# Performance work log

Hardware: AMD Instinct MI355X
Metric: run time of the kernel (lower is better)

## Reference

```python
import jax, jax.numpy as jnp
import numpy as np

ALPHA_F, GAMMA_F = 0.25, 2.0   # focal loss params
SMOOTH = 1e-6                  # dice smooth
THETA = 5.0                    # boundary weight
W_FOCAL, W_DICE, W_BOUND = 0.3, 0.4, 0.3


def _erode(m):
    # one iteration of scipy binary_erosion, cross (connectivity-1) structure,
    # border_value=0 (outside treated as False)
    p = jnp.pad(m, ((0, 0), (0, 0), (1, 1), (1, 1)), constant_values=False)
    c = p[:, :, 1:-1, 1:-1]
    up = p[:, :, :-2, 1:-1]
    dn = p[:, :, 2:, 1:-1]
    lf = p[:, :, 1:-1, :-2]
    rt = p[:, :, 1:-1, 2:]
    return c & up & dn & lf & rt


def _dilate(m):
    # one iteration of scipy binary_dilation, cross structure, border_value=0
    p = jnp.pad(m, ((0, 0), (0, 0), (1, 1), (1, 1)), constant_values=False)
    c = p[:, :, 1:-1, 1:-1]
    up = p[:, :, :-2, 1:-1]
    dn = p[:, :, 2:, 1:-1]
    lf = p[:, :, 1:-1, :-2]
    rt = p[:, :, 1:-1, 2:]
    return c | up | dn | lf | rt


def setup_inputs() -> dict:
    key = jax.random.key(0)
    k1, k2 = jax.random.split(key)
    B, C, H, W = 64, 1, 512, 512
    inputs = jax.random.normal(k1, (B, C, H, W), dtype=jnp.float32)
    targets = jax.random.randint(k2, (B, C, H, W), 0, 2).astype(jnp.float32)
    return {"inputs": inputs, "targets": targets}


def reference(inputs, targets):
    # numerically stable BCE-with-logits, elementwise
    bce = jnp.maximum(inputs, 0.0) - inputs * targets + jnp.log1p(jnp.exp(-jnp.abs(inputs)))

    # --- focal loss ---
    pt = jnp.exp(-bce)
    focal_loss = jnp.mean(ALPHA_F * (1.0 - pt) ** GAMMA_F * bce)

    # --- dice loss ---
    p = jax.nn.sigmoid(inputs)
    intersection = jnp.sum(p * targets)
    dice = (2.0 * intersection + SMOOTH) / (jnp.sum(p) + jnp.sum(targets) + SMOOTH)
    dice_loss = 1.0 - dice

    # --- boundary-weighted BCE ---
    mask = targets > 0.5
    eroded = _erode(_erode(mask))      # iterations=2
    dilated = _dilate(_dilate(mask))   # iterations=2
    boundary = dilated & (~eroded)
    weights = boundary.astype(jnp.float32) * THETA + 1.0
    boundary_loss = jnp.mean(bce * weights)

    return W_FOCAL * focal_loss + W_DICE * dice_loss + W_BOUND * boundary_loss
```

## Files before the change

### kernel.cpp

```cpp
#include <hip/hip_runtime.h>
#include <math.h>

static constexpr int Hdim = 512;
static constexpr int Wdim = 512;
static constexpr int HW   = Hdim * Wdim;
static constexpr int NIMG = 64;
static constexpr int WPR  = Wdim / 64;
static constexpr int WPI  = Hdim * WPR;
static constexpr int TOTAL_WORDS = NIMG * WPI;
static constexpr int NBLK_A = 2048;
static constexpr int GROUPS_PER_WAVE = 8;
static constexpr int NBLK_B = TOTAL_WORDS / 256;
static constexpr int NBLK_C = 2048;
static constexpr int CTHREADS = NBLK_C * 256;
static constexpr int F4TOTAL = NIMG * HW / 4;
static constexpr int CITERS = F4TOTAL / CTHREADS;


typedef unsigned long long ull;

__device__ __forceinline__ ull spread4(ull x) {
    x = (x | (x << 24)) & 0x000000FF000000FFULL;
    x = (x | (x << 12)) & 0x000F000F000F000FULL;
    x = (x | (x << 6))  & 0x0303030303030303ULL;
    x = (x | (x << 3))  & 0x1111111111111111ULL;
    return x;
}

__global__ __launch_bounds__(256) void mask_kernel(
    const float* __restrict__ tgt, ull* __restrict__ mask)
{
    const int lane = threadIdx.x & 63;
    const int wid  = (blockIdx.x * 256 + threadIdx.x) >> 6;
    const float4* t4 = (const float4*)tgt;
    #pragma unroll
    for (int g = 0; g < GROUPS_PER_WAVE; g++) {
        const int gg = wid * GROUPS_PER_WAVE + g;
        float4 v = t4[gg * 64 + lane];
        ull b0 = __ballot(v.x > 0.5f);
        ull b1 = __ballot(v.y > 0.5f);
        ull b2 = __ballot(v.z > 0.5f);
        ull b3 = __ballot(v.w > 0.5f);
        ull w0 =  spread4( b0        & 0xFFFF)       | (spread4( b1        & 0xFFFF) << 1)
               | (spread4( b2        & 0xFFFF) << 2) | (spread4( b3        & 0xFFFF) << 3);
        ull w1 =  spread4((b0 >> 16) & 0xFFFF)       | (spread4((b1 >> 16) & 0xFFFF) << 1)
               | (spread4((b2 >> 16) & 0xFFFF) << 2) | (spread4((b3 >> 16) & 0xFFFF) << 3);
        ull w2 =  spread4((b0 >> 32) & 0xFFFF)       | (spread4((b1 >> 32) & 0xFFFF) << 1)
               | (spread4((b2 >> 32) & 0xFFFF) << 2) | (spread4((b3 >> 32) & 0xFFFF) << 3);
        ull w3 =  spread4((b0 >> 48) & 0xFFFF)       | (spread4((b1 >> 48) & 0xFFFF) << 1)
               | (spread4((b2 >> 48) & 0xFFFF) << 2) | (spread4((b3 >> 48) & 0xFFFF) << 3);
        if (lane < 4) {
            ull val = (lane == 0) ? w0 : (lane == 1) ? w1 : (lane == 2) ? w2 : w3;
            mask[gg * 4 + lane] = val;
        }
    }
}

__device__ __forceinline__ ull shl1(ull c, ull l) { return (c << 1) | (l >> 63); }
__device__ __forceinline__ ull shr1(ull c, ull r) { return (c >> 1) | (r << 63); }
__device__ __forceinline__ ull shl2(ull c, ull l) { return (c << 2) | (l >> 62); }
__device__ __forceinline__ ull shr2(ull c, ull r) { return (c >> 2) | (r << 62); }

__global__ __launch_bounds__(256) void boundary_kernel(
    const ull* __restrict__ mask, ull* __restrict__ comb)
{
    const int w = blockIdx.x * 256 + threadIdx.x;
    const int word = w & 7;
    const int row  = (w >> 3) & (Hdim - 1);
    const ull* mi = mask + (w & ~(WPI - 1));

    #define FW(r, c) ((((unsigned)(r)) < (unsigned)Hdim && ((unsigned)(c)) < (unsigned)WPR) \
                        ? mi[((r) << 3) + (c)] : 0ULL)
    ull c0  = FW(row,     word);
    ull l0  = FW(row,     word - 1);
    ull rr0 = FW(row,     word + 1);
    ull cm  = FW(row - 1, word);
    ull lm  = FW(row - 1, word - 1);
    ull rm  = FW(row - 1, word + 1);
    ull cp  = FW(row + 1, word);
    ull lp  = FW(row + 1, word - 1);
    ull rp  = FW(row + 1, word + 1);
    ull cm2 = FW(row - 2, word);
    ull cp2 = FW(row + 2, word);
    #undef FW

    ull er =
        c0 & shl1(c0,l0) & shr1(c0,rr0) & shl2(c0,l0) & shr2(c0,rr0)
           & cm & shl1(cm,lm) & shr1(cm,rm)
           & cp & shl1(cp,lp) & shr1(cp,rp)
           & cm2 & cp2;
    ull di =
        c0 | shl1(c0,l0) | shr1(c0,rr0) | shl2(c0,l0) | shr2(c0,rr0)
           | cm | shl1(cm,lm) | shr1(cm,rm)
           | cp | shl1(cp,lp) | shr1(cp,rp)
           | cm2 | cp2;

    comb[2 * w]     = c0;
    comb[2 * w + 1] = di & ~er;
}

__global__ __launch_bounds__(256, 4) void combined_loss_kernel(
    const float* __restrict__ inp, const ulonglong2* __restrict__ comb,
    float* __restrict__ partials)
{
    const int tid = blockIdx.x * 256 + threadIdx.x;
    float s_focal = 0.f, s_inter = 0.f, s_p = 0.f, s_bw = 0.f;
    int s_tc = 0;

    #pragma unroll
    for (int it = 0; it < CITERS; it++) {
        const int f4 = tid + it * CTHREADS;
        const float4 v = ((const float4*)inp)[f4];
        const int wi = f4 >> 4;
        const int sh = (f4 & 15) * 4;
        const ulonglong2 cb = comb[wi];
        unsigned int tb4 = (unsigned int)((cb.x >> sh) & 0xFULL);
        unsigned int bb4 = (unsigned int)((cb.y >> sh) & 0xFULL);
        s_tc += __popc(tb4);
        const float xs[4] = {v.x, v.y, v.z, v.w};
        #pragma unroll
        for (int k = 0; k < 4; k++) {
            float xi = xs[k];
            bool tpos = (tb4 >> k) & 1;
            float e  = __expf(-fabsf(xi));
            float bce = fmaxf(xi, 0.f) - (tpos ? xi : 0.f) + __logf(1.f + e);
            float rden = __builtin_amdgcn_rcpf(1.f + e);
            float p = (xi >= 0.f ? 1.f : e) * rden;
            float pt = tpos ? p : 1.f - p;
            float om = 1.f - pt;
            s_focal += 0.25f * om * om * bce;
            s_p     += p;
            s_inter += tpos ? p : 0.f;
            float wgt = ((bb4 >> k) & 1) ? 6.0f : 1.0f;
            s_bw += bce * wgt;
        }
    }
    float s_t = (float)s_tc;

    __shared__ float smem[4][5];
    const int wave = threadIdx.x >> 6;
    const int lane = threadIdx.x & 63;
    #pragma unroll
    for (int off = 32; off > 0; off >>= 1) {
        s_focal += __shfl_down(s_focal, off);
        s_inter += __shfl_down(s_inter, off);
        s_p     += __shfl_down(s_p,     off);
        s_t     += __shfl_down(s_t,     off);
        s_bw    += __shfl_down(s_bw,    off);
    }
    if (lane == 0) {
        smem[wave][0] = s_focal; smem[wave][1] = s_inter; smem[wave][2] = s_p;
        smem[wave][3] = s_t;     smem[wave][4] = s_bw;
    }
    __syncthreads();
    if (threadIdx.x < 5) {
        float a = smem[0][threadIdx.x] + smem[1][threadIdx.x]
                + smem[2][threadIdx.x] + smem[3][threadIdx.x];
        partials[blockIdx.x * 8 + threadIdx.x] = a;
    }
}

__global__ __launch_bounds__(256) void finalize_kernel(
    const float* __restrict__ partials, float* __restrict__ out)
{
    __shared__ float smem[4][5];
    float a0 = 0.f, a1 = 0.f, a2 = 0.f, a3 = 0.f, a4 = 0.f;
    for (int b = threadIdx.x; b < NBLK_C; b += 256) {
        const float* s = partials + b * 8;
        a0 += s[0]; a1 += s[1]; a2 += s[2]; a3 += s[3]; a4 += s[4];
    }
    #pragma unroll
    for (int off = 32; off > 0; off >>= 1) {
        a0 += __shfl_down(a0, off);
        a1 += __shfl_down(a1, off);
        a2 += __shfl_down(a2, off);
        a3 += __shfl_down(a3, off);
        a4 += __shfl_down(a4, off);
    }
    int wave = threadIdx.x >> 6;
    int lane = threadIdx.x & 63;
    if (lane == 0) {
        smem[wave][0] = a0; smem[wave][1] = a1; smem[wave][2] = a2;
        smem[wave][3] = a3; smem[wave][4] = a4;
    }
    __syncthreads();
    if (threadIdx.x == 0) {
        double b0 = 0, b1 = 0, b2 = 0, b3 = 0, b4 = 0;
        #pragma unroll
        for (int w = 0; w < 4; w++) {
            b0 += smem[w][0]; b1 += smem[w][1]; b2 += smem[w][2];
            b3 += smem[w][3]; b4 += smem[w][4];
        }
        double invN = 1.0 / (double)(NIMG * HW);
        double focal_loss = b0 * invN;
        double dice = (2.0 * b1 + 1e-6) / (b2 + b3 + 1e-6);
        double boundary_loss = b4 * invN;
        out[0] = (float)(0.3 * focal_loss + 0.4 * (1.0 - dice) + 0.3 * boundary_loss);
    }
}

extern "C" void kernel_launch(void* const* d_in, const int* in_sizes, int n_in,
                              void* d_out, int out_size, void* d_ws, size_t ws_size,
                              hipStream_t stream) {
    const float* inp = (const float*)d_in[0];
    const float* tgt = (const float*)d_in[1];
    float* out = (float*)d_out;
    char* ws = (char*)d_ws;
    float* partials = (float*)ws;
    ull* tmask = (ull*)(ws + (1u << 20));
    ull* comb  = (ull*)(ws + (4u << 20));

    mask_kernel<<<NBLK_A, 256, 0, stream>>>(tgt, tmask);
    boundary_kernel<<<NBLK_B, 256, 0, stream>>>(tmask, comb);
    combined_loss_kernel<<<NBLK_C, 256, 0, stream>>>(inp, (const ulonglong2*)comb, partials);
    finalize_kernel<<<1, 256, 0, stream>>>(partials, out);
}
```

Baseline: 172.1 us.

## Store target mask as ballot planes and emit per-float4 byte codes

The mask kernel now writes raw ballot bit-planes (one 64-bit word per float4 component) with a single lane, dropping the spread4 bit interleaving. The boundary kernel works directly on these planes, building horizontal neighbours from plane rotations and vertical neighbours from rows ±2, with one thread per 256-pixel group. It then writes a byte per float4 that packs 4 target bits and 4 boundary bits. The loss kernel reads one byte per float4 instead of a 16-byte pair plus shifts, which cuts load traffic and index arithmetic in the hot loop. In exchange the boundary kernel does more bit-shuffling work per thread and runs with fewer threads.

```diff
diff --git a/kernel.cpp b/kernel.cpp
--- a/kernel.cpp
+++ b/kernel.cpp
@@ -5,12 +5,12 @@
 static constexpr int Wdim = 512;
 static constexpr int HW   = Hdim * Wdim;
 static constexpr int NIMG = 64;
-static constexpr int WPR  = Wdim / 64;
-static constexpr int WPI  = Hdim * WPR;
-static constexpr int TOTAL_WORDS = NIMG * WPI;
+static constexpr int GPR  = Wdim / 256;
+static constexpr int GPI  = Hdim * GPR;
+static constexpr int NGRP = NIMG * GPI;
 static constexpr int NBLK_A = 2048;
 static constexpr int GROUPS_PER_WAVE = 8;
-static constexpr int NBLK_B = TOTAL_WORDS / 256;
+static constexpr int NBLK_B = NGRP / 256;
 static constexpr int NBLK_C = 2048;
 static constexpr int CTHREADS = NBLK_C * 256;
 static constexpr int F4TOTAL = NIMG * HW / 4;
@@ -19,14 +19,6 @@
 
 typedef unsigned long long ull;
 
-__device__ __forceinline__ ull spread4(ull x) {
-    x = (x | (x << 24)) & 0x000000FF000000FFULL;
-    x = (x | (x << 12)) & 0x000F000F000F000FULL;
-    x = (x | (x << 6))  & 0x0303030303030303ULL;
-    x = (x | (x << 3))  & 0x1111111111111111ULL;
-    return x;
-}
-
 __global__ __launch_bounds__(256) void mask_kernel(
     const float* __restrict__ tgt, ull* __restrict__ mask)
 {
@@ -37,70 +29,117 @@
     for (int g = 0; g < GROUPS_PER_WAVE; g++) {
         const int gg = wid * GROUPS_PER_WAVE + g;
         float4 v = t4[gg * 64 + lane];
-        ull b0 = __ballot(v.x > 0.5f);
-        ull b1 = __ballot(v.y > 0.5f);
-        ull b2 = __ballot(v.z > 0.5f);
-        ull b3 = __ballot(v.w > 0.5f);
-        ull w0 =  spread4( b0        & 0xFFFF)       | (spread4( b1        & 0xFFFF) << 1)
-               | (spread4( b2        & 0xFFFF) << 2) | (spread4( b3        & 0xFFFF) << 3);
-        ull w1 =  spread4((b0 >> 16) & 0xFFFF)       | (spread4((b1 >> 16) & 0xFFFF) << 1)
-               | (spread4((b2 >> 16) & 0xFFFF) << 2) | (spread4((b3 >> 16) & 0xFFFF) << 3);
-        ull w2 =  spread4((b0 >> 32) & 0xFFFF)       | (spread4((b1 >> 32) & 0xFFFF) << 1)
-               | (spread4((b2 >> 32) & 0xFFFF) << 2) | (spread4((b3 >> 32) & 0xFFFF) << 3);
-        ull w3 =  spread4((b0 >> 48) & 0xFFFF)       | (spread4((b1 >> 48) & 0xFFFF) << 1)
-               | (spread4((b2 >> 48) & 0xFFFF) << 2) | (spread4((b3 >> 48) & 0xFFFF) << 3);
-        if (lane < 4) {
-            ull val = (lane == 0) ? w0 : (lane == 1) ? w1 : (lane == 2) ? w2 : w3;
-            mask[gg * 4 + lane] = val;
-        }
-    }
-}
-
-__device__ __forceinline__ ull shl1(ull c, ull l) { return (c << 1) | (l >> 63); }
-__device__ __forceinline__ ull shr1(ull c, ull r) { return (c >> 1) | (r << 63); }
-__device__ __forceinline__ ull shl2(ull c, ull l) { return (c << 2) | (l >> 62); }
-__device__ __forceinline__ ull shr2(ull c, ull r) { return (c >> 2) | (r << 62); }
+        ull p0 = __ballot(v.x > 0.5f);
+        ull p1 = __ballot(v.y > 0.5f);
+        ull p2 = __ballot(v.z > 0.5f);
+        ull p3 = __ballot(v.w > 0.5f);
+        if (lane == 0) {
+            ulonglong2* mp = (ulonglong2*)(mask + gg * 4);
+            ulonglong2 a; a.x = p0; a.y = p1;
+            ulonglong2 b; b.x = p2; b.y = p3;
+            mp[0] = a;
+            mp[1] = b;
+        }
+    }
+}
+
+__device__ __forceinline__ ull spread8(ull x) {
+    x = (x | (x << 28)) & 0x0000000F0000000FULL;
+    x = (x | (x << 14)) & 0x0003000300030003ULL;
+    x = (x | (x << 7))  & 0x0101010101010101ULL;
+    return x;
+}
+
+struct PlaneRow { ull p0, p1, p2, p3, lc2, lc3, rc0, rc1; };
 
 __global__ __launch_bounds__(256) void boundary_kernel(
-    const ull* __restrict__ mask, ull* __restrict__ comb)
-{
-    const int w = blockIdx.x * 256 + threadIdx.x;
-    const int word = w & 7;
-    const int row  = (w >> 3) & (Hdim - 1);
-    const ull* mi = mask + (w & ~(WPI - 1));
-
-    #define FW(r, c) ((((unsigned)(r)) < (unsigned)Hdim && ((unsigned)(c)) < (unsigned)WPR) \
-                        ? mi[((r) << 3) + (c)] : 0ULL)
-    ull c0  = FW(row,     word);
-    ull l0  = FW(row,     word - 1);
-    ull rr0 = FW(row,     word + 1);
-    ull cm  = FW(row - 1, word);
-    ull lm  = FW(row - 1, word - 1);
-    ull rm  = FW(row - 1, word + 1);
-    ull cp  = FW(row + 1, word);
-    ull lp  = FW(row + 1, word - 1);
-    ull rp  = FW(row + 1, word + 1);
-    ull cm2 = FW(row - 2, word);
-    ull cp2 = FW(row + 2, word);
-    #undef FW
-
-    ull er =
-        c0 & shl1(c0,l0) & shr1(c0,rr0) & shl2(c0,l0) & shr2(c0,rr0)
-           & cm & shl1(cm,lm) & shr1(cm,rm)
-           & cp & shl1(cp,lp) & shr1(cp,rp)
-           & cm2 & cp2;
-    ull di =
-        c0 | shl1(c0,l0) | shr1(c0,rr0) | shl2(c0,l0) | shr2(c0,rr0)
-           | cm | shl1(cm,lm) | shr1(cm,rm)
-           | cp | shl1(cp,lp) | shr1(cp,rp)
-           | cm2 | cp2;
-
-    comb[2 * w]     = c0;
-    comb[2 * w + 1] = di & ~er;
+    const ull* __restrict__ mask, ull* __restrict__ combq)
+{
+    const int gg   = blockIdx.x * 256 + threadIdx.x;
+    const int img  = gg >> 10;
+    const int gi   = gg & (GPI - 1);
+    const int row  = gi >> 1;
+    const int side = gi & 1;
+    const ull* ib = mask + img * GPI * 4;
+
+    PlaneRow pr[5];
+    #pragma unroll
+    for (int d = 0; d < 5; d++) {
+        int rho = row + d - 2;
+        PlaneRow P;
+        if ((unsigned)rho < (unsigned)Hdim) {
+            const ull* ob = ib + (rho * GPR + side) * 4;
+            ulonglong2 a = ((const ulonglong2*)ob)[0];
+            ulonglong2 b = ((const ulonglong2*)ob)[1];
+            P.p0 = a.x; P.p1 = a.y; P.p2 = b.x; P.p3 = b.y;
+            if (side == 1) {
+                const ull* lb = ib + (rho * GPR + 0) * 4;
+                ulonglong2 c = ((const ulonglong2*)lb)[1];
+                P.lc2 = c.x; P.lc3 = c.y;
+            } else { P.lc2 = 0; P.lc3 = 0; }
+            if (side == 0) {
+                const ull* rb = ib + (rho * GPR + 1) * 4;
+                ulonglong2 c = ((const ulonglong2*)rb)[0];
+                P.rc0 = c.x; P.rc1 = c.y;
+            } else { P.rc0 = 0; P.rc1 = 0; }
+        } else {
+            P.p0 = P.p1 = P.p2 = P.p3 = 0; P.lc2 = P.lc3 = 0; P.rc0 = P.rc1 = 0;
+        }
+        pr[d] = P;
+    }
+
+    ull Aa[3][4], Ao[3][4];
+    #pragma unroll
+    for (int j = 0; j < 3; j++) {
+        const PlaneRow& P = pr[j + 1];
+        ull m0 = (P.p3 << 1) | (P.lc3 >> 63);
+        ull m3 = (P.p0 >> 1) | (P.rc0 << 63);
+        Aa[j][0] = P.p0 & P.p1 & m0;  Ao[j][0] = P.p0 | P.p1 | m0;
+        Aa[j][1] = P.p1 & P.p2 & P.p0; Ao[j][1] = P.p1 | P.p2 | P.p0;
+        Aa[j][2] = P.p2 & P.p3 & P.p1; Ao[j][2] = P.p2 | P.p3 | P.p1;
+        Aa[j][3] = P.p3 & m3 & P.p2;  Ao[j][3] = P.p3 | m3 | P.p2;
+    }
+    ull Ba[4], Bo[4];
+    {
+        const PlaneRow& P = pr[2];
+        ull b0m = (P.p2 << 1) | (P.lc2 >> 63);
+        ull b1m = (P.p3 << 1) | (P.lc3 >> 63);
+        ull b2m = (P.p0 >> 1) | (P.rc0 << 63);
+        ull b3m = (P.p1 >> 1) | (P.rc1 << 63);
+        Ba[0] = P.p2 & b0m;  Bo[0] = P.p2 | b0m;
+        Ba[1] = P.p3 & b1m;  Bo[1] = P.p3 | b1m;
+        Ba[2] = P.p0 & b2m;  Bo[2] = P.p0 | b2m;
+        Ba[3] = P.p1 & b3m;  Bo[3] = P.p1 | b3m;
+    }
+    const ull Cm2[4] = { pr[0].p0, pr[0].p1, pr[0].p2, pr[0].p3 };
+    const ull Cp2[4] = { pr[4].p0, pr[4].p1, pr[4].p2, pr[4].p3 };
+    const ull T[4]   = { pr[2].p0, pr[2].p1, pr[2].p2, pr[2].p3 };
+
+    ull B[4];
+    #pragma unroll
+    for (int k = 0; k < 4; k++) {
+        ull er = Aa[0][k] & Aa[1][k] & Aa[2][k] & Ba[k] & Cm2[k] & Cp2[k];
+        ull di = Ao[0][k] | Ao[1][k] | Ao[2][k] | Bo[k] | Cm2[k] | Cp2[k];
+        B[k] = di & ~er;
+    }
+
+    ull* outp = combq + gg * 8;
+    #pragma unroll
+    for (int q = 0; q < 8; q++) {
+        ull o = spread8((T[0] >> (8 * q)) & 0xFF)
+              | (spread8((T[1] >> (8 * q)) & 0xFF) << 1)
+              | (spread8((T[2] >> (8 * q)) & 0xFF) << 2)
+              | (spread8((T[3] >> (8 * q)) & 0xFF) << 3)
+              | (spread8((B[0] >> (8 * q)) & 0xFF) << 4)
+              | (spread8((B[1] >> (8 * q)) & 0xFF) << 5)
+              | (spread8((B[2] >> (8 * q)) & 0xFF) << 6)
+              | (spread8((B[3] >> (8 * q)) & 0xFF) << 7);
+        outp[q] = o;
+    }
 }
 
 __global__ __launch_bounds__(256, 4) void combined_loss_kernel(
-    const float* __restrict__ inp, const ulonglong2* __restrict__ comb,
+    const float* __restrict__ inp, const unsigned char* __restrict__ comb8,
     float* __restrict__ partials)
 {
     const int tid = blockIdx.x * 256 + threadIdx.x;
@@ -111,11 +150,9 @@
     for (int it = 0; it < CITERS; it++) {
         const int f4 = tid + it * CTHREADS;
         const float4 v = ((const float4*)inp)[f4];
-        const int wi = f4 >> 4;
-        const int sh = (f4 & 15) * 4;
-        const ulonglong2 cb = comb[wi];
-        unsigned int tb4 = (unsigned int)((cb.x >> sh) & 0xFULL);
-        unsigned int bb4 = (unsigned int)((cb.y >> sh) & 0xFULL);
+        const unsigned int c = comb8[f4];
+        const unsigned int tb4 = c & 0xF;
+        const unsigned int bb4 = c >> 4;
         s_tc += __popc(tb4);
         const float xs[4] = {v.x, v.y, v.z, v.w};
         #pragma unroll
@@ -207,11 +244,11 @@
     float* out = (float*)d_out;
     char* ws = (char*)d_ws;
     float* partials = (float*)ws;
-    ull* tmask = (ull*)(ws + (1u << 20));
-    ull* comb  = (ull*)(ws + (4u << 20));
-
-    mask_kernel<<<NBLK_A, 256, 0, stream>>>(tgt, tmask);
-    boundary_kernel<<<NBLK_B, 256, 0, stream>>>(tmask, comb);
-    combined_loss_kernel<<<NBLK_C, 256, 0, stream>>>(inp, (const ulonglong2*)comb, partials);
+    ull* mask  = (ull*)(ws + (1u << 20));
+    ull* combq = (ull*)(ws + (4u << 20));
+
+    mask_kernel<<<NBLK_A, 256, 0, stream>>>(tgt, mask);
+    boundary_kernel<<<NBLK_B, 256, 0, stream>>>(mask, combq);
+    combined_loss_kernel<<<NBLK_C, 256, 0, stream>>>(inp, (const unsigned char*)combq, partials);
     finalize_kernel<<<1, 256, 0, stream>>>(partials, out);
 }
```

New measurement: 153.8 us. -10.6%, faster.
